# Optimization experiments

Measured on AMD Instinct MI355X. Metric: run time of the kernel, lower is better.

Reference implementation:

```python
import jax, jax.numpy as jnp
import numpy as np

EPS = 1e-5


def setup_inputs() -> dict:
    key = jax.random.key(0)
    ks = jax.random.split(key, 9)
    B, Cin, C, N, H, W = 8, 512, 256, 19, 128, 128
    return {
        "feat_ffm": jax.random.normal(ks[0], (B, Cin, H, W), dtype=jnp.float32),
        "coarse_x": jax.random.normal(ks[1], (B, N, H, W), dtype=jnp.float32),
        "conv1_w": jax.random.normal(ks[2], (C, Cin), dtype=jnp.float32) * (1.0 / np.sqrt(Cin)),
        "bn_gamma": jax.random.normal(ks[3], (C,), dtype=jnp.float32) * 0.1 + 1.0,
        "bn_beta": jax.random.normal(ks[4], (C,), dtype=jnp.float32) * 0.1,
        "bn_mean": jax.random.normal(ks[5], (C,), dtype=jnp.float32) * 0.1,
        "bn_var": jax.random.uniform(ks[6], (C,), dtype=jnp.float32, minval=0.5, maxval=1.5),
        "conv2_w": jax.random.normal(ks[7], (C, C), dtype=jnp.float32) * (1.0 / np.sqrt(C)),
        "conv2_b": jax.random.normal(ks[8], (C,), dtype=jnp.float32) * 0.01,
    }


def reference(feat_ffm, coarse_x, conv1_w, bn_gamma, bn_beta, bn_mean, bn_var, conv2_w, conv2_b):
    # conv1: 1x1 conv (no bias) + BatchNorm (eval) + ReLU; Dropout2d is identity in eval.
    feat = jnp.einsum('bihw,oi->bohw', feat_ffm, conv1_w)          # [B,C,H,W]
    scale = bn_gamma / jnp.sqrt(bn_var + EPS)                      # [C]
    bias = bn_beta - bn_mean * scale
    feat = jax.nn.relu(feat * scale[None, :, None, None] + bias[None, :, None, None])

    B, N, H, W = coarse_x.shape
    C = feat.shape[1]
    q = coarse_x.reshape(B, N, H * W)                              # proj_query [B,N,HW]
    k = feat.reshape(B, C, H * W)                                  # proj_key^T is [B,HW,C]
    energy = jnp.einsum('bns,bcs->bnc', q, k)                      # [B,N,C]
    attn = jax.nn.softmax(energy, axis=-1)                         # softmax over C
    out = jnp.einsum('bnc,bns->bcs', attn, q)                      # attn^T @ value -> [B,C,HW]
    out = out.reshape(B, C, H, W)
    out = jnp.einsum('bihw,oi->bohw', out, conv2_w) + conv2_b[None, :, None, None]
    return out
```

## Files before the change

### kernel.cpp

```cpp
#include <hip/hip_runtime.h>

typedef __attribute__((ext_vector_type(8))) _Float16 f16x8;
typedef __attribute__((ext_vector_type(4))) float f32x4;
typedef __attribute__((ext_vector_type(2))) float f32x2;

#define MFMA16(A, Bv, Cv) __builtin_amdgcn_mfma_f32_16x16x32_f16(A, Bv, Cv, 0, 0, 0)

#define NB 8
#define CIN 512
#define NC 256
#define NQ 19

#define WS_WH 0
#define WS_WL 262144
#define WS_W2T 524288
#define WS_BIAS 786432
#define WS_M 787456

__global__ __launch_bounds__(256) void k_prep(
    const float* __restrict__ w1, const float* __restrict__ gamma,
    const float* __restrict__ beta, const float* __restrict__ mean,
    const float* __restrict__ var, const float* __restrict__ w2,
    char* __restrict__ ws) {
  _Float16* wh = (_Float16*)(ws + WS_WH);
  _Float16* wl = (_Float16*)(ws + WS_WL);
  float* w2t = (float*)(ws + WS_W2T);
  float* bias = (float*)(ws + WS_BIAS);
  const int bid = blockIdx.x, t = threadIdx.x;
  if (bid < 128) {
    for (int u = 0; u < 4; ++u) {
      int e = bid * 1024 + u * 256 + t;
      int j = e & 7, l6 = (e >> 3) & 63, mfq = (e >> 9) & 15, kk = e >> 13;
      int c = mfq * 16 + (l6 & 15);
      int k = kk * 32 + (l6 >> 4) * 8 + j;
      float sc = gamma[c] / sqrtf(var[c] + 1e-5f);
      float wf = w1[c * 512 + k] * sc * 32.0f;
      _Float16 h = (_Float16)wf;
      wh[e] = h;
      wl[e] = (_Float16)(wf - (float)h);
    }
  } else if (bid < 192) {
    for (int u = 0; u < 4; ++u) {
      int e = (bid - 128) * 1024 + u * 256 + t;
      int i = e >> 8, o = e & 255;
      w2t[e] = w2[o * 256 + i];
    }
  } else {
    float sc = gamma[t] / sqrtf(var[t] + 1e-5f);
    bias[t] = beta[t] - mean[t] * sc;
  }
}

__global__ __launch_bounds__(256, 2) void k_conv1_energy(
    const float* __restrict__ x, const float* __restrict__ qx,
    const char* __restrict__ ws, float* __restrict__ part) {
  __shared__ __align__(16) char smem[53248];
  const int tid = threadIdx.x;
  const int l = tid & 63, w = tid >> 6;
  const int a = l & 15, g = l >> 4;
  const int h = w & 1;
  const int bid = blockIdx.x;
  const int sblk = bid & 127, b = bid >> 7;
  const int s0 = (sblk << 7) + ((w >> 1) << 6);

  const f16x8* __restrict__ whv = (const f16x8*)(ws + WS_WH);
  const f16x8* __restrict__ wlv = (const f16x8*)(ws + WS_WL);

  const float* __restrict__ xb = x + (((size_t)(b * CIN)) << 14) + s0 + a;

  f32x4 acc[8][4];
  const f32x4 zz = {0.f, 0.f, 0.f, 0.f};
  #pragma unroll
  for (int i = 0; i < 8; ++i)
    #pragma unroll
    for (int j = 0; j < 4; ++j) acc[i][j] = zz;

  float xr[4][8];
  #pragma unroll
  for (int nf = 0; nf < 4; ++nf)
    #pragma unroll
    for (int j = 0; j < 8; ++j)
      xr[nf][j] = xb[((size_t)(g * 8 + j) << 14) + nf * 16];

  f16x8 ah[2], al[2];

  #pragma unroll 1
  for (int kk = 0; kk < 16; ++kk) {
    #pragma unroll
    for (int m2 = 0; m2 < 2; ++m2) {
      int aidx = (kk * 16 + h * 8 + m2) * 64 + l;
      ah[m2] = whv[aidx];
      al[m2] = wlv[aidx];
    }
    f16x8 bh[4], bl[4];
    #pragma unroll
    for (int nf = 0; nf < 4; ++nf)
      #pragma unroll
      for (int j = 0; j < 8; ++j) {
        float v = xr[nf][j] * 32.f;
        _Float16 hi = (_Float16)v;
        bh[nf][j] = hi;
        bl[nf][j] = (_Float16)(v - (float)hi);
      }
    if (kk < 15) {
      #pragma unroll
      for (int nf = 0; nf < 4; ++nf)
        #pragma unroll
        for (int j = 0; j < 8; ++j)
          xr[nf][j] = xb[((size_t)((kk + 1) * 32 + g * 8 + j) << 14) + nf * 16];
    }
    #pragma unroll
    for (int mf = 0; mf < 8; ++mf) {
      f16x8 cah = ah[mf & 1], cal = al[mf & 1];
      #pragma unroll
      for (int nf = 0; nf < 4; ++nf) {
        acc[mf][nf] = MFMA16(cah, bh[nf], acc[mf][nf]);
        acc[mf][nf] = MFMA16(cal, bh[nf], acc[mf][nf]);
        acc[mf][nf] = MFMA16(cah, bl[nf], acc[mf][nf]);
      }
      if (mf < 6) {
        int aidx = (kk * 16 + h * 8 + mf + 2) * 64 + l;
        ah[mf & 1] = whv[aidx];
        al[mf & 1] = wlv[aidx];
      }
    }
  }

  {
    const float* __restrict__ biasg = (const float*)(ws + WS_BIAS);
    #pragma unroll
    for (int mf = 0; mf < 8; ++mf)
      #pragma unroll
      for (int r4 = 0; r4 < 4; ++r4) {
        float bi = biasg[h * 128 + mf * 16 + g * 4 + r4];
        #pragma unroll
        for (int nf = 0; nf < 4; ++nf)
          acc[mf][nf][r4] = fmaxf(acc[mf][nf][r4] * (1.0f / 1024.0f) + bi, 0.f);
      }
  }

  float ea0[19], ea1[19];
  #pragma unroll
  for (int n = 0; n < 19; ++n) { ea0[n] = 0.f; ea1[n] = 0.f; }
  float* kvq = (float*)(smem + w * 8448);
  const float* __restrict__ qb = qx + (((size_t)(b * NQ)) << 14) + s0;

  #pragma unroll
  for (int nf = 0; nf < 4; ++nf) {
    #pragma unroll
    for (int mf = 0; mf < 8; ++mf)
      *(f32x4*)&kvq[a * 132 + mf * 16 + g * 4] = acc[mf][nf];
    asm volatile("s_waitcnt lgkmcnt(0)" ::: "memory");
    __builtin_amdgcn_sched_barrier(0);
    #pragma unroll
    for (int spc = 0; spc < 4; ++spc) {
      float4 qv[19];
      #pragma unroll
      for (int n = 0; n < 19; ++n)
        qv[n] = *(const float4*)(qb + ((size_t)n << 14) + nf * 16 + spc * 4);
      #pragma unroll
      for (int sj = 0; sj < 4; ++sj) {
        float kv0 = kvq[(spc * 4 + sj) * 132 + l];
        float kv1 = kvq[(spc * 4 + sj) * 132 + 64 + l];
        #pragma unroll
        for (int n = 0; n < 19; ++n) {
          float qs = ((const float*)&qv[n])[sj];
          ea0[n] = fmaf(qs, kv0, ea0[n]);
          ea1[n] = fmaf(qs, kv1, ea1[n]);
        }
      }
    }
  }

  float* comb = (float*)(smem + 33792 + h * 9728);
  if (w >= 2) {
    #pragma unroll
    for (int n = 0; n < 19; ++n) {
      comb[n * 128 + l] = ea0[n];
      comb[n * 128 + 64 + l] = ea1[n];
    }
  }
  __syncthreads();
  if (w < 2) {
    float* pp = part + (size_t)bid * (NQ * 256) + h * 128 + l;
    #pragma unroll
    for (int n = 0; n < 19; ++n) {
      pp[n * 256]      = ea0[n] + comb[n * 128 + l];
      pp[n * 256 + 64] = ea1[n] + comb[n * 128 + 64 + l];
    }
  }
}

__global__ __launch_bounds__(256) void k_softmax_m(
    const float* __restrict__ part, const char* __restrict__ ws,
    float* __restrict__ Mout) {
  const int bn = blockIdx.x;
  const int b = bn / 19, n = bn % 19;
  const int t = threadIdx.x;
  const float* __restrict__ w2t = (const float*)(ws + WS_W2T);
  float e = 0.f;
  const float* pp = part + ((size_t)(b * 128) * NQ + n) * 256 + t;
  for (int sb = 0; sb < 128; ++sb)
    e += pp[(size_t)sb * (NQ * 256)];
  __shared__ float sred[4];
  __shared__ float attn_lds[256];
  float m = e;
  #pragma unroll
  for (int d = 1; d < 64; d <<= 1) m = fmaxf(m, __shfl_xor(m, d, 64));
  if ((t & 63) == 0) sred[t >> 6] = m;
  __syncthreads();
  m = fmaxf(fmaxf(sred[0], sred[1]), fmaxf(sred[2], sred[3]));
  float p = __expf(e - m);
  float s = p;
  #pragma unroll
  for (int d = 1; d < 64; d <<= 1) s += __shfl_xor(s, d, 64);
  __syncthreads();
  if ((t & 63) == 0) sred[t >> 6] = s;
  __syncthreads();
  s = sred[0] + sred[1] + sred[2] + sred[3];
  attn_lds[t] = p / s;
  __syncthreads();
  float macc = 0.f;
  #pragma unroll 8
  for (int i = 0; i < 256; ++i)
    macc = fmaf(attn_lds[i], w2t[i * 256 + t], macc);
  Mout[(size_t)bn * 256 + t] = macc;
}

__global__ __launch_bounds__(256, 2) void k_out(
    const float* __restrict__ qx, const float* __restrict__ Mg,
    const float* __restrict__ b2, float* __restrict__ out) {
  const int bid = blockIdx.x;
  const int b = bid >> 6, sc = bid & 63;
  const int s0 = sc * 256;
  const int t = threadIdx.x;
  __shared__ float qlds[19 * 256];
  for (int idx = t; idx < 19 * 256; idx += 256) {
    int n = idx >> 8, s = idx & 255;
    qlds[idx] = qx[((size_t)(b * NQ + n) << 14) + s0 + s];
  }
  __syncthreads();
  const int tg = t >> 4, a2 = (t & 15) * 2;
  #pragma unroll 1
  for (int ocg = 0; ocg < 4; ++ocg) {
    float m[4][19];
    float bi[4];
    #pragma unroll
    for (int oj = 0; oj < 4; ++oj) {
      int o = (ocg * 4 + oj) * 16 + tg;
      bi[oj] = b2[o];
      #pragma unroll
      for (int n = 0; n < 19; ++n)
        m[oj][n] = Mg[((size_t)b * NQ + n) * 256 + o];
    }
    #pragma unroll 1
    for (int sp = 0; sp < 8; ++sp) {
      int s = sp * 32 + a2;
      f32x2 acc2[4];
      #pragma unroll
      for (int oj = 0; oj < 4; ++oj) { acc2[oj].x = bi[oj]; acc2[oj].y = bi[oj]; }
      #pragma unroll
      for (int n = 0; n < 19; ++n) {
        f32x2 q2 = *(const f32x2*)&qlds[n * 256 + s];
        #pragma unroll
        for (int oj = 0; oj < 4; ++oj) {
          acc2[oj].x = fmaf(m[oj][n], q2.x, acc2[oj].x);
          acc2[oj].y = fmaf(m[oj][n], q2.y, acc2[oj].y);
        }
      }
      #pragma unroll
      for (int oj = 0; oj < 4; ++oj) {
        int o = (ocg * 4 + oj) * 16 + tg;
        *(f32x2*)&out[((size_t)(b * NC + o) << 14) + s0 + s] = acc2[oj];
      }
    }
  }
}

extern "C" void kernel_launch(void* const* d_in, const int* in_sizes, int n_in,
                              void* d_out, int out_size, void* d_ws, size_t ws_size,
                              hipStream_t stream) {
  const float* x     = (const float*)d_in[0];
  const float* cx    = (const float*)d_in[1];
  const float* w1    = (const float*)d_in[2];
  const float* gamma = (const float*)d_in[3];
  const float* beta  = (const float*)d_in[4];
  const float* mean  = (const float*)d_in[5];
  const float* var   = (const float*)d_in[6];
  const float* w2    = (const float*)d_in[7];
  const float* b2    = (const float*)d_in[8];
  char* ws = (char*)d_ws;
  float* out = (float*)d_out;
  float* part = (float*)d_out;
  float* Mptr = (float*)(ws + WS_M);

  k_prep<<<193, 256, 0, stream>>>(w1, gamma, beta, mean, var, w2, ws);
  k_conv1_energy<<<1024, 256, 0, stream>>>(x, cx, ws, part);
  k_softmax_m<<<152, 256, 0, stream>>>(part, ws, Mptr);
  k_out<<<512, 256, 0, stream>>>(cx, Mptr, b2, out);
}
```

Before: 238.8 us.

## Stage conv1 x and weight tiles through LDS via global_load_lds DMA

Restructures the conv1+energy kernel into 512-thread blocks covering 256 spatial positions. Each k-step's x slab and the interleaved hi/lo fp16 weight tile are loaded into LDS with asynchronous global_load_lds, and the next step's DMA is issued while the MFMAs run. Weights are repacked so the hi and lo halves of a k-step are contiguous. The in-block combine of spatial halves is removed, so each wave pair writes its own partials and the softmax reduction loop doubles to 256 partials. The goal is to cut redundant global weight reads and improve load coalescing, at the cost of more barriers, larger LDS use and more partial-sum traffic.

Measured after the change: 239.6 us. About the same (+0.3%).

```diff
diff --git a/kernel.cpp b/kernel.cpp
--- a/kernel.cpp
+++ b/kernel.cpp
@@ -11,8 +11,7 @@
 #define NC 256
 #define NQ 19
 
-#define WS_WH 0
-#define WS_WL 262144
+#define WS_WA 0
 #define WS_W2T 524288
 #define WS_BIAS 786432
 #define WS_M 787456
@@ -22,22 +21,23 @@
     const float* __restrict__ beta, const float* __restrict__ mean,
     const float* __restrict__ var, const float* __restrict__ w2,
     char* __restrict__ ws) {
-  _Float16* wh = (_Float16*)(ws + WS_WH);
-  _Float16* wl = (_Float16*)(ws + WS_WL);
+  _Float16* wa = (_Float16*)(ws + WS_WA);
   float* w2t = (float*)(ws + WS_W2T);
   float* bias = (float*)(ws + WS_BIAS);
   const int bid = blockIdx.x, t = threadIdx.x;
   if (bid < 128) {
-    for (int u = 0; u < 4; ++u) {
-      int e = bid * 1024 + u * 256 + t;
-      int j = e & 7, l6 = (e >> 3) & 63, mfq = (e >> 9) & 15, kk = e >> 13;
-      int c = mfq * 16 + (l6 & 15);
-      int k = kk * 32 + (l6 >> 4) * 8 + j;
+    for (int u = 0; u < 8; ++u) {
+      int i = bid * 2048 + u * 256 + t;
+      int kk = i >> 14, r = i & 16383;
+      int half = r >> 13, q = r & 8191;
+      int mfq = q >> 9, s = q & 511;
+      int l = s >> 3, j = s & 7;
+      int c = mfq * 16 + (l & 15);
+      int k = kk * 32 + (l >> 4) * 8 + j;
       float sc = gamma[c] / sqrtf(var[c] + 1e-5f);
       float wf = w1[c * 512 + k] * sc * 32.0f;
       _Float16 h = (_Float16)wf;
-      wh[e] = h;
-      wl[e] = (_Float16)(wf - (float)h);
+      wa[i] = half ? (_Float16)(wf - (float)h) : h;
     }
   } else if (bid < 192) {
     for (int u = 0; u < 4; ++u) {
@@ -51,22 +51,21 @@
   }
 }
 
-__global__ __launch_bounds__(256, 2) void k_conv1_energy(
+__global__ __launch_bounds__(512, 2) void k_conv1_energy(
     const float* __restrict__ x, const float* __restrict__ qx,
     const char* __restrict__ ws, float* __restrict__ part) {
-  __shared__ __align__(16) char smem[53248];
+  __shared__ __align__(16) char smem[67584];
   const int tid = threadIdx.x;
   const int l = tid & 63, w = tid >> 6;
   const int a = l & 15, g = l >> 4;
-  const int h = w & 1;
+  const int h = w & 1, sq = w >> 1;
   const int bid = blockIdx.x;
-  const int sblk = bid & 127, b = bid >> 7;
-  const int s0 = (sblk << 7) + ((w >> 1) << 6);
-
-  const f16x8* __restrict__ whv = (const f16x8*)(ws + WS_WH);
-  const f16x8* __restrict__ wlv = (const f16x8*)(ws + WS_WL);
-
-  const float* __restrict__ xb = x + (((size_t)(b * CIN)) << 14) + s0 + a;
+  const int sblk = bid & 63, b = bid >> 6;
+  const int s0 = sblk << 8;
+
+  const char* __restrict__ wsA = ws + WS_WA;
+  char* const smemA = smem + 33280;
+  const float* __restrict__ xg = x + (((size_t)(b * CIN)) << 14) + s0;
 
   f32x4 acc[8][4];
   const f32x4 zz = {0.f, 0.f, 0.f, 0.f};
@@ -75,75 +74,101 @@
     #pragma unroll
     for (int j = 0; j < 4; ++j) acc[i][j] = zz;
 
-  float xr[4][8];
-  #pragma unroll
-  for (int nf = 0; nf < 4; ++nf)
-    #pragma unroll
-    for (int j = 0; j < 8; ++j)
-      xr[nf][j] = xb[((size_t)(g * 8 + j) << 14) + nf * 16];
-
-  f16x8 ah[2], al[2];
+#define DMA_STEP(KK) do {                                                      \
+    _Pragma("unroll") for (int i_ = 0; i_ < 4; ++i_) {                         \
+      int row_ = w * 4 + i_;                                                   \
+      const float* src_ = xg + (((size_t)((KK) * 32 + row_)) << 14) + l * 4;   \
+      __builtin_amdgcn_global_load_lds((const unsigned int*)src_,              \
+          (unsigned int*)&smem[row_ * 1040], 16, 0, 0);                        \
+    }                                                                          \
+    _Pragma("unroll") for (int i_ = 0; i_ < 4; ++i_) {                         \
+      int ch_ = w * 4 + i_;                                                    \
+      const char* srcA_ = wsA + (KK) * 32768 + ch_ * 1024 + l * 16;            \
+      __builtin_amdgcn_global_load_lds((const unsigned int*)srcA_,             \
+          (unsigned int*)&smemA[ch_ * 1024], 16, 0, 0);                        \
+    }                                                                          \
+  } while (0)
+
+  DMA_STEP(0);
+  asm volatile("s_waitcnt vmcnt(0)" ::: "memory");
+  __builtin_amdgcn_sched_barrier(0);
+  __builtin_amdgcn_s_barrier();
+  __builtin_amdgcn_sched_barrier(0);
 
   #pragma unroll 1
   for (int kk = 0; kk < 16; ++kk) {
-    #pragma unroll
-    for (int m2 = 0; m2 < 2; ++m2) {
-      int aidx = (kk * 16 + h * 8 + m2) * 64 + l;
-      ah[m2] = whv[aidx];
-      al[m2] = wlv[aidx];
+    f16x8 ah[8], al[8];
+    #pragma unroll
+    for (int mf = 0; mf < 8; ++mf) {
+      ah[mf] = *(const f16x8*)&smemA[(h * 8 + mf) * 1024 + l * 16];
+      al[mf] = *(const f16x8*)&smemA[16384 + (h * 8 + mf) * 1024 + l * 16];
     }
     f16x8 bh[4], bl[4];
     #pragma unroll
-    for (int nf = 0; nf < 4; ++nf)
+    for (int nf = 0; nf < 4; ++nf) {
+      const int scol = (sq * 64 + nf * 16 + a) * 4;
+      float xr[8];
+      #pragma unroll
+      for (int j = 0; j < 8; ++j)
+        xr[j] = *(const float*)&smem[(g * 8 + j) * 1040 + scol];
       #pragma unroll
       for (int j = 0; j < 8; ++j) {
-        float v = xr[nf][j] * 32.f;
-        _Float16 hi = (_Float16)v;
-        bh[nf][j] = hi;
-        bl[nf][j] = (_Float16)(v - (float)hi);
-      }
+        float v = xr[j] * 32.f;
+        _Float16 hh = (_Float16)v;
+        bh[nf][j] = hh;
+        bl[nf][j] = (_Float16)(v - (float)hh);
+      }
+    }
+    asm volatile("s_waitcnt lgkmcnt(0)" ::: "memory");
+    __builtin_amdgcn_sched_barrier(0);
+    __builtin_amdgcn_s_barrier();
+    __builtin_amdgcn_sched_barrier(0);
+    if (kk < 15) DMA_STEP(kk + 1);
+    __builtin_amdgcn_s_setprio(1);
+    #pragma unroll
+    for (int nf = 0; nf < 4; ++nf) {
+      #pragma unroll
+      for (int mf = 0; mf < 8; ++mf)
+        acc[mf][nf] = MFMA16(ah[mf], bh[nf], acc[mf][nf]);
+      #pragma unroll
+      for (int mf = 0; mf < 8; ++mf)
+        acc[mf][nf] = MFMA16(al[mf], bh[nf], acc[mf][nf]);
+      #pragma unroll
+      for (int mf = 0; mf < 8; ++mf)
+        acc[mf][nf] = MFMA16(ah[mf], bl[nf], acc[mf][nf]);
+    }
+    __builtin_amdgcn_s_setprio(0);
     if (kk < 15) {
-      #pragma unroll
-      for (int nf = 0; nf < 4; ++nf)
-        #pragma unroll
-        for (int j = 0; j < 8; ++j)
-          xr[nf][j] = xb[((size_t)((kk + 1) * 32 + g * 8 + j) << 14) + nf * 16];
-    }
-    #pragma unroll
-    for (int mf = 0; mf < 8; ++mf) {
-      f16x8 cah = ah[mf & 1], cal = al[mf & 1];
-      #pragma unroll
-      for (int nf = 0; nf < 4; ++nf) {
-        acc[mf][nf] = MFMA16(cah, bh[nf], acc[mf][nf]);
-        acc[mf][nf] = MFMA16(cal, bh[nf], acc[mf][nf]);
-        acc[mf][nf] = MFMA16(cah, bl[nf], acc[mf][nf]);
-      }
-      if (mf < 6) {
-        int aidx = (kk * 16 + h * 8 + mf + 2) * 64 + l;
-        ah[mf & 1] = whv[aidx];
-        al[mf & 1] = wlv[aidx];
-      }
-    }
-  }
+      asm volatile("s_waitcnt vmcnt(0)" ::: "memory");
+      __builtin_amdgcn_sched_barrier(0);
+      __builtin_amdgcn_s_barrier();
+      __builtin_amdgcn_sched_barrier(0);
+    }
+  }
+
+  __syncthreads();
 
   {
     const float* __restrict__ biasg = (const float*)(ws + WS_BIAS);
     #pragma unroll
-    for (int mf = 0; mf < 8; ++mf)
+    for (int mf = 0; mf < 8; ++mf) {
+      const float4 bq = *(const float4*)(biasg + h * 128 + mf * 16 + g * 4);
       #pragma unroll
       for (int r4 = 0; r4 < 4; ++r4) {
-        float bi = biasg[h * 128 + mf * 16 + g * 4 + r4];
+        float bi = ((const float*)&bq)[r4];
         #pragma unroll
         for (int nf = 0; nf < 4; ++nf)
           acc[mf][nf][r4] = fmaxf(acc[mf][nf][r4] * (1.0f / 1024.0f) + bi, 0.f);
       }
+    }
   }
 
   float ea0[19], ea1[19];
   #pragma unroll
   for (int n = 0; n < 19; ++n) { ea0[n] = 0.f; ea1[n] = 0.f; }
   float* kvq = (float*)(smem + w * 8448);
-  const float* __restrict__ qb = qx + (((size_t)(b * NQ)) << 14) + s0;
+  const float* __restrict__ qb =
+      qx + (((size_t)(b * NQ)) << 14) + s0 + (sq << 6);
 
   #pragma unroll
   for (int nf = 0; nf < 4; ++nf) {
@@ -172,22 +197,11 @@
     }
   }
 
-  float* comb = (float*)(smem + 33792 + h * 9728);
-  if (w >= 2) {
-    #pragma unroll
-    for (int n = 0; n < 19; ++n) {
-      comb[n * 128 + l] = ea0[n];
-      comb[n * 128 + 64 + l] = ea1[n];
-    }
-  }
-  __syncthreads();
-  if (w < 2) {
-    float* pp = part + (size_t)bid * (NQ * 256) + h * 128 + l;
-    #pragma unroll
-    for (int n = 0; n < 19; ++n) {
-      pp[n * 256]      = ea0[n] + comb[n * 128 + l];
-      pp[n * 256 + 64] = ea1[n] + comb[n * 128 + 64 + l];
-    }
+  float* pp = part + (size_t)(bid * 4 + sq) * (NQ * 256) + h * 128 + l;
+  #pragma unroll
+  for (int n = 0; n < 19; ++n) {
+    pp[n * 256] = ea0[n];
+    pp[n * 256 + 64] = ea1[n];
   }
 }
 
@@ -199,8 +213,8 @@
   const int t = threadIdx.x;
   const float* __restrict__ w2t = (const float*)(ws + WS_W2T);
   float e = 0.f;
-  const float* pp = part + ((size_t)(b * 128) * NQ + n) * 256 + t;
-  for (int sb = 0; sb < 128; ++sb)
+  const float* pp = part + ((size_t)(b * 256) * NQ + n) * 256 + t;
+  for (int sb = 0; sb < 256; ++sb)
     e += pp[(size_t)sb * (NQ * 256)];
   __shared__ float sred[4];
   __shared__ float attn_lds[256];
@@ -295,7 +309,7 @@
   float* Mptr = (float*)(ws + WS_M);
 
   k_prep<<<193, 256, 0, stream>>>(w1, gamma, beta, mean, var, w2, ws);
-  k_conv1_energy<<<1024, 256, 0, stream>>>(x, cx, ws, part);
+  k_conv1_energy<<<512, 512, 0, stream>>>(x, cx, ws, part);
   k_softmax_m<<<152, 256, 0, stream>>>(part, ws, Mptr);
   k_out<<<512, 256, 0, stream>>>(cx, Mptr, b2, out);
 }
```
